# Performance work log

Measured on AMD Instinct MI355X. Metric: run time of the kernel, lower is better.

Reference implementation:

```python
import jax, jax.numpy as jnp
import numpy as np


def setup_inputs() -> dict:
    key = jax.random.key(0)
    ks = jax.random.split(key, 8)
    B, M, C, H, W = 2, 16, 256, 64, 64
    T = 1024  # transformer_dim
    return {
        "transformer_output": jax.random.normal(ks[0], (B, T), dtype=jnp.float32),
        "residual_maps": jax.random.normal(ks[1], (B, M, C, H, W), dtype=jnp.float32),
        "Wq": jax.random.normal(ks[2], (C, T), dtype=jnp.float32) * 0.02,
        "bq": jnp.zeros((C,), dtype=jnp.float32),
        "Wk": jax.random.normal(ks[3], (C, C), dtype=jnp.float32) * 0.02,
        "bk": jnp.zeros((C,), dtype=jnp.float32),
        "Wv": jax.random.normal(ks[4], (C, C), dtype=jnp.float32) * 0.02,
        "bv": jnp.zeros((C,), dtype=jnp.float32),
    }


def reference(transformer_output, residual_maps, Wq, bq, Wk, bk, Wv, bv):
    # residual_maps: [B, M, C, H, W]; single query per batch element.
    B, M, C, H, W = residual_maps.shape
    scale = C ** (-0.5)
    # Linear query projection: [B, C]
    q = transformer_output @ Wq.T + bq
    # 1x1 conv == per-pixel channel matmul: [B, M, C, H, W]
    keys = jnp.einsum("oc,bmchw->bmohw", Wk, residual_maps) + bk[None, None, :, None, None]
    values = jnp.einsum("oc,bmchw->bmohw", Wv, residual_maps) + bv[None, None, :, None, None]
    # Single-query dot-product scores per (map, pixel): [B, M, H, W]
    scores = jnp.einsum("bc,bmchw->bmhw", q, keys) * scale
    # Temporal softmax over num_maps at each spatial position
    probs = jax.nn.softmax(scores, axis=1)
    # Softmax-weighted sum of value maps: [B, C, H, W]
    out = jnp.einsum("bmhw,bmchw->bchw", probs, values)
    return out
```

## Files before the change

### kernel.cpp

```cpp
#include <hip/hip_runtime.h>

#define SCALE 0.0625f
#define ROW 36

typedef __attribute__((ext_vector_type(4))) float f32x4;
typedef __attribute__((ext_vector_type(8))) short s16x8;
typedef __attribute__((ext_vector_type(8))) unsigned short u16x8;

__device__ __forceinline__ unsigned short f2bf(float x) {
    unsigned u = __float_as_uint(x);
    u = u + 0x7FFF + ((u >> 16) & 1);
    return (unsigned short)(u >> 16);
}

__global__ __launch_bounds__(256) void prep1_kernel(
    const float* __restrict__ TO,
    const float* __restrict__ Wq,
    const float* __restrict__ bq,
    const float* __restrict__ Wv,
    float* __restrict__ qbuf,
    unsigned short* __restrict__ WvB)
{
    const int blk = blockIdx.x;
    const int t   = threadIdx.x;
    if (blk < 16) {
        const int b    = blk >> 3;
        const int rblk = blk & 7;
        const int wv = t >> 6, l = t & 63;
        const float4* Wq4 = (const float4*)Wq;
        const float4* TO4 = (const float4*)TO;
        for (int rr = 0; rr < 8; ++rr) {
            const int c = rblk * 32 + wv * 8 + rr;
            float acc = 0.f;
#pragma unroll
            for (int i = 0; i < 4; ++i) {
                float4 wq = Wq4[c * 256 + i * 64 + l];
                float4 tv = TO4[b * 256 + i * 64 + l];
                acc = fmaf(wq.x, tv.x, acc);
                acc = fmaf(wq.y, tv.y, acc);
                acc = fmaf(wq.z, tv.z, acc);
                acc = fmaf(wq.w, tv.w, acc);
            }
#pragma unroll
            for (int mask = 1; mask < 64; mask <<= 1)
                acc += __shfl_xor(acc, mask, 64);
            if (l == 0) qbuf[b * 256 + c] = acc + bq[c];
        }
    } else {
        const int idx = blk - 16;
#pragma unroll
        for (int i = 0; i < 4; ++i) {
            const int e = idx * 4096 + i * 1024 + t * 4;
            const float4 f = ((const float4*)Wv)[e >> 2];
            ushort4 o;
            o.x = f2bf(f.x); o.y = f2bf(f.y);
            o.z = f2bf(f.z); o.w = f2bf(f.w);
            *(ushort4*)(WvB + e) = o;
        }
    }
}

__global__ __launch_bounds__(256) void prep2_kernel(
    const float* __restrict__ qbuf,
    const float* __restrict__ Wk,
    float* __restrict__ qks)
{
    const int blk = blockIdx.x;
    const int t   = threadIdx.x;
    const int b = blk >> 3, j = blk & 7;
    const int col = t & 31, chunk = t >> 5;
    const int cp = j * 32 + col;
    float partial = 0.f;
#pragma unroll 8
    for (int cc = 0; cc < 32; ++cc) {
        const int c = chunk * 32 + cc;
        partial = fmaf(qbuf[b * 256 + c], Wk[c * 256 + cp], partial);
    }
    __shared__ float r2[8][32];
    r2[chunk][col] = partial;
    __syncthreads();
    if (t < 32) {
        float s = 0.f;
#pragma unroll
        for (int k = 0; k < 8; ++k) s += r2[k][t];
        qks[b * 256 + j * 32 + t] = SCALE * s;
    }
}

__global__ __launch_bounds__(512) void score_kernel(
    const float* __restrict__ X,
    const float* __restrict__ qks,
    float* __restrict__ Sp)
{
    const int blk = blockIdx.x;
    const int ch  = blk & 7;
    const int bm  = blk >> 3;
    const int b   = bm >> 4;
    const int t   = threadIdx.x;
    const int c0  = ch * 32;
    const float4* X4 = (const float4*)X;
    const int base = (bm * 256 + c0) * 1024;

    float4 a0 = make_float4(0.f, 0.f, 0.f, 0.f);
    float4 a1 = make_float4(0.f, 0.f, 0.f, 0.f);
#pragma unroll 4
    for (int c = 0; c < 32; ++c) {
        const float q = qks[b * 256 + c0 + c];
        const float4 x0 = X4[base + c * 1024 + t];
        const float4 x1 = X4[base + c * 1024 + t + 512];
        a0.x = fmaf(q, x0.x, a0.x); a0.y = fmaf(q, x0.y, a0.y);
        a0.z = fmaf(q, x0.z, a0.z); a0.w = fmaf(q, x0.w, a0.w);
        a1.x = fmaf(q, x1.x, a1.x); a1.y = fmaf(q, x1.y, a1.y);
        a1.z = fmaf(q, x1.z, a1.z); a1.w = fmaf(q, x1.w, a1.w);
    }
    float4* S4 = (float4*)(Sp + (ch * 32 + bm) * 4096);
    S4[t]       = a0;
    S4[t + 512] = a1;
}

__global__ __launch_bounds__(128) void softmax_kernel(
    const float* __restrict__ Sp,
    float* __restrict__ P)
{
    const int blk = blockIdx.x;
    const int b   = blk >> 5;
    const int px  = ((blk & 31) << 7) + threadIdx.x;
    float e[16];
    float sum = 0.f;
#pragma unroll
    for (int m = 0; m < 16; ++m) {
        float s = 0.f;
#pragma unroll
        for (int ch = 0; ch < 8; ++ch)
            s += Sp[((ch * 2 + b) * 16 + m) * 4096 + px];
        e[m] = __expf(s);
        sum += e[m];
    }
    const float inv = 1.0f / sum;
#pragma unroll
    for (int m = 0; m < 16; ++m)
        P[(b * 16 + m) * 4096 + px] = e[m] * inv;
}

__global__ __launch_bounds__(512) void wsum_kernel(
    const float* __restrict__ X,
    const float* __restrict__ P,
    unsigned short* __restrict__ Ybf)
{
    const int blk = blockIdx.x;
    const int ph  = blk & 1;
    const int oc  = (blk >> 1) & 63;
    const int b   = blk >> 7;
    const int t   = threadIdx.x;
    const int o0  = oc * 4;
    const int px4 = (ph << 9) + t;
    const float4* X4 = (const float4*)X;
    const float4* P4 = (const float4*)P;

    float4 acc[4];
#pragma unroll
    for (int o = 0; o < 4; ++o) acc[o] = make_float4(0.f, 0.f, 0.f, 0.f);

#pragma unroll 2
    for (int m = 0; m < 16; ++m) {
        const float4 p = P4[(b * 16 + m) * 1024 + px4];
#pragma unroll
        for (int o = 0; o < 4; ++o) {
            const float4 x = X4[((b * 16 + m) * 256 + o0 + o) * 1024 + px4];
            acc[o].x = fmaf(p.x, x.x, acc[o].x);
            acc[o].y = fmaf(p.y, x.y, acc[o].y);
            acc[o].z = fmaf(p.z, x.z, acc[o].z);
            acc[o].w = fmaf(p.w, x.w, acc[o].w);
        }
    }
#pragma unroll
    for (int o = 0; o < 4; ++o) {
        ushort4 y;
        y.x = f2bf(acc[o].x); y.y = f2bf(acc[o].y);
        y.z = f2bf(acc[o].z); y.w = f2bf(acc[o].w);
        *(ushort4*)(Ybf + (b * 256 + o0 + o) * 4096 + px4 * 4) = y;
    }
}

__global__ __launch_bounds__(512) void conv_kernel(
    const unsigned short* __restrict__ Ybf,
    const unsigned short* __restrict__ WvB,
    const float* __restrict__ bv,
    float* __restrict__ out)
{
    const int blk = blockIdx.x;
    const int b   = blk >> 7;
    const int px0 = (blk & 127) << 5;
    const int t   = threadIdx.x;
    const int lane = t & 63;
    const int w    = t >> 6;

    __shared__ float slab[256 * ROW];

    {
        const int o = t >> 2, q = t & 3;
#pragma unroll
        for (int h = 0; h < 2; ++h) {
            const int oo = o + h * 128;
            const u16x8 v = *(const u16x8*)(Ybf + (b * 256 + oo) * 4096 + px0 + q * 8);
#pragma unroll
            for (int j = 0; j < 8; ++j)
                slab[oo * ROW + q * 8 + j] =
                    __uint_as_float((unsigned)(unsigned short)v[j] << 16);
        }
    }
    __syncthreads();

    const int px16 = lane & 15;
    const int quad = lane >> 4;

    f32x4 acc[2][2];
#pragma unroll
    for (int tl = 0; tl < 2; ++tl)
#pragma unroll
        for (int pxh = 0; pxh < 2; ++pxh)
#pragma unroll
            for (int r = 0; r < 4; ++r)
                acc[tl][pxh][r] = bv[16 * (w * 2 + tl) + quad * 4 + r];

#pragma unroll
    for (int ks = 0; ks < 8; ++ks) {
        s16x8 bfr[2];
#pragma unroll
        for (int pxh = 0; pxh < 2; ++pxh)
#pragma unroll
            for (int j = 0; j < 8; ++j)
                bfr[pxh][j] = (short)f2bf(
                    slab[(ks * 32 + quad * 8 + j) * ROW + pxh * 16 + px16]);
#pragma unroll
        for (int tl = 0; tl < 2; ++tl) {
            const s16x8 afr = *(const s16x8*)(
                WvB + (16 * (w * 2 + tl) + px16) * 256 + ks * 32 + quad * 8);
#pragma unroll
            for (int pxh = 0; pxh < 2; ++pxh)
                acc[tl][pxh] = __builtin_amdgcn_mfma_f32_16x16x32_bf16(
                    afr, bfr[pxh], acc[tl][pxh], 0, 0, 0);
        }
    }

    const int obase = b * 256 * 4096 + px0;
#pragma unroll
    for (int tl = 0; tl < 2; ++tl)
#pragma unroll
        for (int pxh = 0; pxh < 2; ++pxh)
#pragma unroll
            for (int r = 0; r < 4; ++r) {
                const int co = 16 * (w * 2 + tl) + quad * 4 + r;
                out[obase + co * 4096 + pxh * 16 + px16] = acc[tl][pxh][r];
            }
}

extern "C" void kernel_launch(void* const* d_in, const int* in_sizes, int n_in,
                              void* d_out, int out_size, void* d_ws, size_t ws_size,
                              hipStream_t stream) {
    const float* TO = (const float*)d_in[0];
    const float* X  = (const float*)d_in[1];
    const float* Wq = (const float*)d_in[2];
    const float* bq = (const float*)d_in[3];
    const float* Wk = (const float*)d_in[4];
    const float* Wv = (const float*)d_in[6];
    const float* bv = (const float*)d_in[7];
    float* out = (float*)d_out;
    float* ws  = (float*)d_ws;

    float*          qbuf = ws;
    float*          qks  = ws + 512;
    unsigned short* WvB  = (unsigned short*)(ws + 1024);
    float*          Sp   = ws + 33792;
    float*          P    = ws + 1082368;
    unsigned short* Ybf  = (unsigned short*)(ws + 1213440);

    hipLaunchKernelGGL(prep1_kernel, dim3(32), dim3(256), 0, stream,
                       TO, Wq, bq, Wv, qbuf, WvB);
    hipLaunchKernelGGL(prep2_kernel, dim3(16), dim3(256), 0, stream,
                       qbuf, Wk, qks);
    hipLaunchKernelGGL(score_kernel, dim3(256), dim3(512), 0, stream,
                       X, qks, Sp);
    hipLaunchKernelGGL(softmax_kernel, dim3(64), dim3(128), 0, stream,
                       Sp, P);
    hipLaunchKernelGGL(wsum_kernel, dim3(256), dim3(512), 0, stream,
                       X, P, Ybf);
    hipLaunchKernelGGL(conv_kernel, dim3(256), dim3(512), 0, stream,
                       Ybf, WvB, bv, out);
}
```

Before: 248.9 us.

## Fuse five stage kernels into one cooperative kernel with grid syncs

Replaces the prep2, score, softmax, wsum and conv launches with a single cooperative kernel of 256 blocks that separates the stages with grid.sync barriers. The softmax stage is also rewritten to use float4 loads and a shuffle reduction over the 16 maps, spread across 32 blocks of 512 threads instead of 64 blocks of 128. This removes per-launch overhead and inter-kernel gaps. In exchange it adds grid-wide barrier costs, leaves most blocks idle during the small stages, and needs all 256 blocks to be co-resident. The large shared slab now sits in every block for the whole kernel, which may limit occupancy.

```diff
diff --git a/kernel.cpp b/kernel.cpp
--- a/kernel.cpp
+++ b/kernel.cpp
@@ -1,4 +1,7 @@
 #include <hip/hip_runtime.h>
+#include <hip/hip_cooperative_groups.h>
+
+namespace cg = cooperative_groups;
 
 #define SCALE 0.0625f
 #define ROW 36
@@ -60,199 +63,206 @@
     }
 }
 
-__global__ __launch_bounds__(256) void prep2_kernel(
+__global__ __launch_bounds__(512, 2) void fused_kernel(
+    const float* __restrict__ X,
     const float* __restrict__ qbuf,
     const float* __restrict__ Wk,
-    float* __restrict__ qks)
-{
-    const int blk = blockIdx.x;
-    const int t   = threadIdx.x;
-    const int b = blk >> 3, j = blk & 7;
-    const int col = t & 31, chunk = t >> 5;
-    const int cp = j * 32 + col;
-    float partial = 0.f;
-#pragma unroll 8
-    for (int cc = 0; cc < 32; ++cc) {
-        const int c = chunk * 32 + cc;
-        partial = fmaf(qbuf[b * 256 + c], Wk[c * 256 + cp], partial);
-    }
-    __shared__ float r2[8][32];
-    r2[chunk][col] = partial;
-    __syncthreads();
-    if (t < 32) {
-        float s = 0.f;
-#pragma unroll
-        for (int k = 0; k < 8; ++k) s += r2[k][t];
-        qks[b * 256 + j * 32 + t] = SCALE * s;
-    }
-}
-
-__global__ __launch_bounds__(512) void score_kernel(
-    const float* __restrict__ X,
-    const float* __restrict__ qks,
-    float* __restrict__ Sp)
-{
-    const int blk = blockIdx.x;
-    const int ch  = blk & 7;
-    const int bm  = blk >> 3;
-    const int b   = bm >> 4;
-    const int t   = threadIdx.x;
-    const int c0  = ch * 32;
-    const float4* X4 = (const float4*)X;
-    const int base = (bm * 256 + c0) * 1024;
-
-    float4 a0 = make_float4(0.f, 0.f, 0.f, 0.f);
-    float4 a1 = make_float4(0.f, 0.f, 0.f, 0.f);
-#pragma unroll 4
-    for (int c = 0; c < 32; ++c) {
-        const float q = qks[b * 256 + c0 + c];
-        const float4 x0 = X4[base + c * 1024 + t];
-        const float4 x1 = X4[base + c * 1024 + t + 512];
-        a0.x = fmaf(q, x0.x, a0.x); a0.y = fmaf(q, x0.y, a0.y);
-        a0.z = fmaf(q, x0.z, a0.z); a0.w = fmaf(q, x0.w, a0.w);
-        a1.x = fmaf(q, x1.x, a1.x); a1.y = fmaf(q, x1.y, a1.y);
-        a1.z = fmaf(q, x1.z, a1.z); a1.w = fmaf(q, x1.w, a1.w);
-    }
-    float4* S4 = (float4*)(Sp + (ch * 32 + bm) * 4096);
-    S4[t]       = a0;
-    S4[t + 512] = a1;
-}
-
-__global__ __launch_bounds__(128) void softmax_kernel(
-    const float* __restrict__ Sp,
-    float* __restrict__ P)
-{
-    const int blk = blockIdx.x;
-    const int b   = blk >> 5;
-    const int px  = ((blk & 31) << 7) + threadIdx.x;
-    float e[16];
-    float sum = 0.f;
-#pragma unroll
-    for (int m = 0; m < 16; ++m) {
-        float s = 0.f;
-#pragma unroll
-        for (int ch = 0; ch < 8; ++ch)
-            s += Sp[((ch * 2 + b) * 16 + m) * 4096 + px];
-        e[m] = __expf(s);
-        sum += e[m];
-    }
-    const float inv = 1.0f / sum;
-#pragma unroll
-    for (int m = 0; m < 16; ++m)
-        P[(b * 16 + m) * 4096 + px] = e[m] * inv;
-}
-
-__global__ __launch_bounds__(512) void wsum_kernel(
-    const float* __restrict__ X,
-    const float* __restrict__ P,
-    unsigned short* __restrict__ Ybf)
-{
-    const int blk = blockIdx.x;
-    const int ph  = blk & 1;
-    const int oc  = (blk >> 1) & 63;
-    const int b   = blk >> 7;
-    const int t   = threadIdx.x;
-    const int o0  = oc * 4;
-    const int px4 = (ph << 9) + t;
-    const float4* X4 = (const float4*)X;
-    const float4* P4 = (const float4*)P;
-
-    float4 acc[4];
-#pragma unroll
-    for (int o = 0; o < 4; ++o) acc[o] = make_float4(0.f, 0.f, 0.f, 0.f);
-
-#pragma unroll 2
-    for (int m = 0; m < 16; ++m) {
-        const float4 p = P4[(b * 16 + m) * 1024 + px4];
-#pragma unroll
-        for (int o = 0; o < 4; ++o) {
-            const float4 x = X4[((b * 16 + m) * 256 + o0 + o) * 1024 + px4];
-            acc[o].x = fmaf(p.x, x.x, acc[o].x);
-            acc[o].y = fmaf(p.y, x.y, acc[o].y);
-            acc[o].z = fmaf(p.z, x.z, acc[o].z);
-            acc[o].w = fmaf(p.w, x.w, acc[o].w);
-        }
-    }
-#pragma unroll
-    for (int o = 0; o < 4; ++o) {
-        ushort4 y;
-        y.x = f2bf(acc[o].x); y.y = f2bf(acc[o].y);
-        y.z = f2bf(acc[o].z); y.w = f2bf(acc[o].w);
-        *(ushort4*)(Ybf + (b * 256 + o0 + o) * 4096 + px4 * 4) = y;
-    }
-}
-
-__global__ __launch_bounds__(512) void conv_kernel(
-    const unsigned short* __restrict__ Ybf,
+    float* __restrict__ qks,
+    float* __restrict__ Sp,
+    float* __restrict__ P,
+    unsigned short* __restrict__ Ybf,
     const unsigned short* __restrict__ WvB,
     const float* __restrict__ bv,
     float* __restrict__ out)
 {
+    cg::grid_group grid = cg::this_grid();
     const int blk = blockIdx.x;
-    const int b   = blk >> 7;
-    const int px0 = (blk & 127) << 5;
     const int t   = threadIdx.x;
-    const int lane = t & 63;
-    const int w    = t >> 6;
 
     __shared__ float slab[256 * ROW];
+    __shared__ float r2[16][32];
+
+    if (blk < 16) {
+        const int b = blk >> 3, j = blk & 7;
+        const int col = t & 31, chunk = t >> 5;
+        const int cp = j * 32 + col;
+        float partial = 0.f;
+#pragma unroll
+        for (int cc = 0; cc < 16; ++cc) {
+            const int c = chunk * 16 + cc;
+            partial = fmaf(qbuf[b * 256 + c], Wk[c * 256 + cp], partial);
+        }
+        r2[chunk][col] = partial;
+        __syncthreads();
+        if (t < 32) {
+            float s = 0.f;
+#pragma unroll
+            for (int k = 0; k < 16; ++k) s += r2[k][t];
+            qks[b * 256 + j * 32 + t] = SCALE * s;
+        }
+    }
+    __threadfence();
+    grid.sync();
 
     {
-        const int o = t >> 2, q = t & 3;
-#pragma unroll
-        for (int h = 0; h < 2; ++h) {
-            const int oo = o + h * 128;
-            const u16x8 v = *(const u16x8*)(Ybf + (b * 256 + oo) * 4096 + px0 + q * 8);
-#pragma unroll
-            for (int j = 0; j < 8; ++j)
-                slab[oo * ROW + q * 8 + j] =
-                    __uint_as_float((unsigned)(unsigned short)v[j] << 16);
-        }
-    }
-    __syncthreads();
-
-    const int px16 = lane & 15;
-    const int quad = lane >> 4;
-
-    f32x4 acc[2][2];
-#pragma unroll
-    for (int tl = 0; tl < 2; ++tl)
-#pragma unroll
-        for (int pxh = 0; pxh < 2; ++pxh)
-#pragma unroll
-            for (int r = 0; r < 4; ++r)
-                acc[tl][pxh][r] = bv[16 * (w * 2 + tl) + quad * 4 + r];
-
-#pragma unroll
-    for (int ks = 0; ks < 8; ++ks) {
-        s16x8 bfr[2];
-#pragma unroll
-        for (int pxh = 0; pxh < 2; ++pxh)
-#pragma unroll
-            for (int j = 0; j < 8; ++j)
-                bfr[pxh][j] = (short)f2bf(
-                    slab[(ks * 32 + quad * 8 + j) * ROW + pxh * 16 + px16]);
-#pragma unroll
-        for (int tl = 0; tl < 2; ++tl) {
-            const s16x8 afr = *(const s16x8*)(
-                WvB + (16 * (w * 2 + tl) + px16) * 256 + ks * 32 + quad * 8);
+        const int ch = blk & 7;
+        const int bm = blk >> 3;
+        const int b  = bm >> 4;
+        const int c0 = ch * 32;
+        const float4* X4 = (const float4*)X;
+        const int base = (bm * 256 + c0) * 1024;
+
+        float4 a0 = make_float4(0.f, 0.f, 0.f, 0.f);
+        float4 a1 = make_float4(0.f, 0.f, 0.f, 0.f);
+#pragma unroll 4
+        for (int c = 0; c < 32; ++c) {
+            const float q = qks[b * 256 + c0 + c];
+            const float4 x0 = X4[base + c * 1024 + t];
+            const float4 x1 = X4[base + c * 1024 + t + 512];
+            a0.x = fmaf(q, x0.x, a0.x); a0.y = fmaf(q, x0.y, a0.y);
+            a0.z = fmaf(q, x0.z, a0.z); a0.w = fmaf(q, x0.w, a0.w);
+            a1.x = fmaf(q, x1.x, a1.x); a1.y = fmaf(q, x1.y, a1.y);
+            a1.z = fmaf(q, x1.z, a1.z); a1.w = fmaf(q, x1.w, a1.w);
+        }
+        float4* S4 = (float4*)(Sp + (ch * 32 + bm) * 4096);
+        S4[t]       = a0;
+        S4[t + 512] = a1;
+    }
+    __threadfence();
+    grid.sync();
+
+    if (blk < 32) {
+        const int b = blk >> 4, g = blk & 15;
+        const int m = t & 15, f4g = t >> 4;
+        const float4* Sp4 = (const float4*)Sp;
+#pragma unroll
+        for (int rep = 0; rep < 2; ++rep) {
+            const int f4c = g * 64 + rep * 32 + f4g;
+            float4 s = make_float4(0.f, 0.f, 0.f, 0.f);
+#pragma unroll
+            for (int ch = 0; ch < 8; ++ch) {
+                const float4 v = Sp4[((ch * 2 + b) * 16 + m) * 1024 + f4c];
+                s.x += v.x; s.y += v.y; s.z += v.z; s.w += v.w;
+            }
+            float4 e;
+            e.x = __expf(s.x); e.y = __expf(s.y);
+            e.z = __expf(s.z); e.w = __expf(s.w);
+            float4 tot = e;
+#pragma unroll
+            for (int mask = 1; mask < 16; mask <<= 1) {
+                tot.x += __shfl_xor(tot.x, mask, 64);
+                tot.y += __shfl_xor(tot.y, mask, 64);
+                tot.z += __shfl_xor(tot.z, mask, 64);
+                tot.w += __shfl_xor(tot.w, mask, 64);
+            }
+            float4 p;
+            p.x = e.x / tot.x; p.y = e.y / tot.y;
+            p.z = e.z / tot.z; p.w = e.w / tot.w;
+            ((float4*)P)[(b * 16 + m) * 1024 + f4c] = p;
+        }
+    }
+    __threadfence();
+    grid.sync();
+
+    {
+        const int ph = blk & 1;
+        const int oc = (blk >> 1) & 63;
+        const int b  = blk >> 7;
+        const int o0 = oc * 4;
+        const int px4 = (ph << 9) + t;
+        const float4* X4 = (const float4*)X;
+        const float4* P4 = (const float4*)P;
+
+        float4 acc[4];
+#pragma unroll
+        for (int o = 0; o < 4; ++o) acc[o] = make_float4(0.f, 0.f, 0.f, 0.f);
+
+#pragma unroll 2
+        for (int m = 0; m < 16; ++m) {
+            const float4 p = P4[(b * 16 + m) * 1024 + px4];
+#pragma unroll
+            for (int o = 0; o < 4; ++o) {
+                const float4 x = X4[((b * 16 + m) * 256 + o0 + o) * 1024 + px4];
+                acc[o].x = fmaf(p.x, x.x, acc[o].x);
+                acc[o].y = fmaf(p.y, x.y, acc[o].y);
+                acc[o].z = fmaf(p.z, x.z, acc[o].z);
+                acc[o].w = fmaf(p.w, x.w, acc[o].w);
+            }
+        }
+#pragma unroll
+        for (int o = 0; o < 4; ++o) {
+            ushort4 y;
+            y.x = f2bf(acc[o].x); y.y = f2bf(acc[o].y);
+            y.z = f2bf(acc[o].z); y.w = f2bf(acc[o].w);
+            *(ushort4*)(Ybf + (b * 256 + o0 + o) * 4096 + px4 * 4) = y;
+        }
+    }
+    __threadfence();
+    grid.sync();
+
+    {
+        const int b   = blk >> 7;
+        const int px0 = (blk & 127) << 5;
+        const int lane = t & 63;
+        const int w    = t >> 6;
+
+        {
+            const int o = t >> 2, q = t & 3;
+#pragma unroll
+            for (int h = 0; h < 2; ++h) {
+                const int oo = o + h * 128;
+                const u16x8 v = *(const u16x8*)(Ybf + (b * 256 + oo) * 4096 + px0 + q * 8);
+#pragma unroll
+                for (int j = 0; j < 8; ++j)
+                    slab[oo * ROW + q * 8 + j] =
+                        __uint_as_float((unsigned)(unsigned short)v[j] << 16);
+            }
+        }
+        __syncthreads();
+
+        const int px16 = lane & 15;
+        const int quad = lane >> 4;
+
+        f32x4 acc[2][2];
+#pragma unroll
+        for (int tl = 0; tl < 2; ++tl)
 #pragma unroll
             for (int pxh = 0; pxh < 2; ++pxh)
-                acc[tl][pxh] = __builtin_amdgcn_mfma_f32_16x16x32_bf16(
-                    afr, bfr[pxh], acc[tl][pxh], 0, 0, 0);
-        }
-    }
-
-    const int obase = b * 256 * 4096 + px0;
-#pragma unroll
-    for (int tl = 0; tl < 2; ++tl)
-#pragma unroll
-        for (int pxh = 0; pxh < 2; ++pxh)
-#pragma unroll
-            for (int r = 0; r < 4; ++r) {
-                const int co = 16 * (w * 2 + tl) + quad * 4 + r;
-                out[obase + co * 4096 + pxh * 16 + px16] = acc[tl][pxh][r];
-            }
+#pragma unroll
+                for (int r = 0; r < 4; ++r)
+                    acc[tl][pxh][r] = bv[16 * (w * 2 + tl) + quad * 4 + r];
+
+#pragma unroll
+        for (int ks = 0; ks < 8; ++ks) {
+            s16x8 bfr[2];
+#pragma unroll
+            for (int pxh = 0; pxh < 2; ++pxh)
+#pragma unroll
+                for (int j = 0; j < 8; ++j)
+                    bfr[pxh][j] = (short)f2bf(
+                        slab[(ks * 32 + quad * 8 + j) * ROW + pxh * 16 + px16]);
+#pragma unroll
+            for (int tl = 0; tl < 2; ++tl) {
+                const s16x8 afr = *(const s16x8*)(
+                    WvB + (16 * (w * 2 + tl) + px16) * 256 + ks * 32 + quad * 8);
+#pragma unroll
+                for (int pxh = 0; pxh < 2; ++pxh)
+                    acc[tl][pxh] = __builtin_amdgcn_mfma_f32_16x16x32_bf16(
+                        afr, bfr[pxh], acc[tl][pxh], 0, 0, 0);
+            }
+        }
+
+        const int obase = b * 256 * 4096 + px0;
+#pragma unroll
+        for (int tl = 0; tl < 2; ++tl)
+#pragma unroll
+            for (int pxh = 0; pxh < 2; ++pxh)
+#pragma unroll
+                for (int r = 0; r < 4; ++r) {
+                    const int co = 16 * (w * 2 + tl) + quad * 4 + r;
+                    out[obase + co * 4096 + pxh * 16 + px16] = acc[tl][pxh][r];
+                }
+    }
 }
 
 extern "C" void kernel_launch(void* const* d_in, const int* in_sizes, int n_in,
@@ -277,14 +287,10 @@
 
     hipLaunchKernelGGL(prep1_kernel, dim3(32), dim3(256), 0, stream,
                        TO, Wq, bq, Wv, qbuf, WvB);
-    hipLaunchKernelGGL(prep2_kernel, dim3(16), dim3(256), 0, stream,
-                       qbuf, Wk, qks);
-    hipLaunchKernelGGL(score_kernel, dim3(256), dim3(512), 0, stream,
-                       X, qks, Sp);
-    hipLaunchKernelGGL(softmax_kernel, dim3(64), dim3(128), 0, stream,
-                       Sp, P);
-    hipLaunchKernelGGL(wsum_kernel, dim3(256), dim3(512), 0, stream,
-                       X, P, Ybf);
-    hipLaunchKernelGGL(conv_kernel, dim3(256), dim3(512), 0, stream,
-                       Ybf, WvB, bv, out);
-}
+
+    void* args[] = {(void*)&X, (void*)&qbuf, (void*)&Wk, (void*)&qks,
+                    (void*)&Sp, (void*)&P, (void*)&Ybf, (void*)&WvB,
+                    (void*)&bv, (void*)&out};
+    hipLaunchCooperativeKernel((const void*)fused_kernel, dim3(256), dim3(512),
+                               args, 0, stream);
+}
```

After: 585.9 us. +135.4%, slower.

## Fuse prep stages, reduce scores in-block, and fold softmax into weighted sum

Applied to the files above, without the earlier changes.

Merges the query projection and Wk folding into one prep kernel that uses shared memory. The score kernel now reduces the channel partials inside each block and writes final scores directly, so the 8x partial-score buffer goes away. Softmax moves into the weighted-sum kernel: each block recomputes the exp and normalisation from the scores, so the softmax launch and the P round trip are removed. This cuts two launches and a lot of intermediate traffic, but the exp work is repeated across the 64 output-channel blocks, and the prep path is now serial in only 2 blocks.

```diff
diff --git a/kernel.cpp b/kernel.cpp
--- a/kernel.cpp
+++ b/kernel.cpp
@@ -13,24 +13,25 @@
     return (unsigned short)(u >> 16);
 }
 
-__global__ __launch_bounds__(256) void prep1_kernel(
+__global__ __launch_bounds__(256) void prep_kernel(
     const float* __restrict__ TO,
     const float* __restrict__ Wq,
     const float* __restrict__ bq,
+    const float* __restrict__ Wk,
     const float* __restrict__ Wv,
-    float* __restrict__ qbuf,
+    float* __restrict__ qks,
     unsigned short* __restrict__ WvB)
 {
     const int blk = blockIdx.x;
     const int t   = threadIdx.x;
-    if (blk < 16) {
-        const int b    = blk >> 3;
-        const int rblk = blk & 7;
+    if (blk < 2) {
+        const int b = blk;
+        __shared__ float sq[256];
         const int wv = t >> 6, l = t & 63;
         const float4* Wq4 = (const float4*)Wq;
         const float4* TO4 = (const float4*)TO;
-        for (int rr = 0; rr < 8; ++rr) {
-            const int c = rblk * 32 + wv * 8 + rr;
+        for (int rr = 0; rr < 64; ++rr) {
+            const int c = wv * 64 + rr;
             float acc = 0.f;
 #pragma unroll
             for (int i = 0; i < 4; ++i) {
@@ -44,10 +45,16 @@
 #pragma unroll
             for (int mask = 1; mask < 64; mask <<= 1)
                 acc += __shfl_xor(acc, mask, 64);
-            if (l == 0) qbuf[b * 256 + c] = acc + bq[c];
-        }
+            if (l == 0) sq[c] = acc + bq[c];
+        }
+        __syncthreads();
+        float val = 0.f;
+#pragma unroll 8
+        for (int c = 0; c < 256; ++c)
+            val = fmaf(sq[c], Wk[c * 256 + t], val);
+        qks[b * 256 + t] = SCALE * val;
     } else {
-        const int idx = blk - 16;
+        const int idx = blk - 2;
 #pragma unroll
         for (int i = 0; i < 4; ++i) {
             const int e = idx * 4096 + i * 1024 + t * 4;
@@ -60,102 +67,78 @@
     }
 }
 
-__global__ __launch_bounds__(256) void prep2_kernel(
-    const float* __restrict__ qbuf,
-    const float* __restrict__ Wk,
-    float* __restrict__ qks)
-{
-    const int blk = blockIdx.x;
-    const int t   = threadIdx.x;
-    const int b = blk >> 3, j = blk & 7;
-    const int col = t & 31, chunk = t >> 5;
-    const int cp = j * 32 + col;
-    float partial = 0.f;
-#pragma unroll 8
-    for (int cc = 0; cc < 32; ++cc) {
-        const int c = chunk * 32 + cc;
-        partial = fmaf(qbuf[b * 256 + c], Wk[c * 256 + cp], partial);
-    }
-    __shared__ float r2[8][32];
-    r2[chunk][col] = partial;
-    __syncthreads();
-    if (t < 32) {
-        float s = 0.f;
-#pragma unroll
-        for (int k = 0; k < 8; ++k) s += r2[k][t];
-        qks[b * 256 + j * 32 + t] = SCALE * s;
-    }
-}
-
-__global__ __launch_bounds__(512) void score_kernel(
+__global__ __launch_bounds__(256, 2) void score_kernel(
     const float* __restrict__ X,
     const float* __restrict__ qks,
-    float* __restrict__ Sp)
-{
-    const int blk = blockIdx.x;
-    const int ch  = blk & 7;
-    const int bm  = blk >> 3;
+    float* __restrict__ S)
+{
+    const int blk = blockIdx.x;
+    const int bm  = blk >> 4;
+    const int pxq = blk & 15;
     const int b   = bm >> 4;
     const int t   = threadIdx.x;
-    const int c0  = ch * 32;
+    const int cg  = t >> 6, f4l = t & 63;
+
     const float4* X4 = (const float4*)X;
-    const int base = (bm * 256 + c0) * 1024;
-
-    float4 a0 = make_float4(0.f, 0.f, 0.f, 0.f);
-    float4 a1 = make_float4(0.f, 0.f, 0.f, 0.f);
-#pragma unroll 4
-    for (int c = 0; c < 32; ++c) {
-        const float q = qks[b * 256 + c0 + c];
-        const float4 x0 = X4[base + c * 1024 + t];
-        const float4 x1 = X4[base + c * 1024 + t + 512];
-        a0.x = fmaf(q, x0.x, a0.x); a0.y = fmaf(q, x0.y, a0.y);
-        a0.z = fmaf(q, x0.z, a0.z); a0.w = fmaf(q, x0.w, a0.w);
-        a1.x = fmaf(q, x1.x, a1.x); a1.y = fmaf(q, x1.y, a1.y);
-        a1.z = fmaf(q, x1.z, a1.z); a1.w = fmaf(q, x1.w, a1.w);
-    }
-    float4* S4 = (float4*)(Sp + (ch * 32 + bm) * 4096);
-    S4[t]       = a0;
-    S4[t + 512] = a1;
-}
-
-__global__ __launch_bounds__(128) void softmax_kernel(
-    const float* __restrict__ Sp,
-    float* __restrict__ P)
-{
-    const int blk = blockIdx.x;
-    const int b   = blk >> 5;
-    const int px  = ((blk & 31) << 7) + threadIdx.x;
-    float e[16];
-    float sum = 0.f;
+    const int base = (bm * 256 + cg * 64) * 1024 + pxq * 64 + f4l;
+    const float* q = qks + b * 256 + cg * 64;
+
+    float4 a = make_float4(0.f, 0.f, 0.f, 0.f);
+#pragma unroll 8
+    for (int cc = 0; cc < 64; ++cc) {
+        const float4 x = X4[base + cc * 1024];
+        const float qv = q[cc];
+        a.x = fmaf(qv, x.x, a.x);
+        a.y = fmaf(qv, x.y, a.y);
+        a.z = fmaf(qv, x.z, a.z);
+        a.w = fmaf(qv, x.w, a.w);
+    }
+    __shared__ float4 part[4][64];
+    part[cg][f4l] = a;
+    __syncthreads();
+    if (t < 64) {
+        const float4 s0 = part[0][t], s1 = part[1][t];
+        const float4 s2 = part[2][t], s3 = part[3][t];
+        float4 r;
+        r.x = s0.x + s1.x + s2.x + s3.x;
+        r.y = s0.y + s1.y + s2.y + s3.y;
+        r.z = s0.z + s1.z + s2.z + s3.z;
+        r.w = s0.w + s1.w + s2.w + s3.w;
+        ((float4*)S)[bm * 1024 + pxq * 64 + t] = r;
+    }
+}
+
+__global__ __launch_bounds__(256, 2) void wsum_kernel(
+    const float* __restrict__ X,
+    const float* __restrict__ S,
+    unsigned short* __restrict__ Ybf)
+{
+    const int blk = blockIdx.x;
+    const int pxq = blk & 3;
+    const int oc  = (blk >> 2) & 63;
+    const int b   = blk >> 8;
+    const int t   = threadIdx.x;
+    const int px4 = pxq * 256 + t;
+    const int o0  = oc * 4;
+    const float4* X4 = (const float4*)X;
+    const float4* S4 = (const float4*)S;
+
+    float4 p[16];
+    float4 tot = make_float4(0.f, 0.f, 0.f, 0.f);
 #pragma unroll
     for (int m = 0; m < 16; ++m) {
-        float s = 0.f;
-#pragma unroll
-        for (int ch = 0; ch < 8; ++ch)
-            s += Sp[((ch * 2 + b) * 16 + m) * 4096 + px];
-        e[m] = __expf(s);
-        sum += e[m];
-    }
-    const float inv = 1.0f / sum;
-#pragma unroll
-    for (int m = 0; m < 16; ++m)
-        P[(b * 16 + m) * 4096 + px] = e[m] * inv;
-}
-
-__global__ __launch_bounds__(512) void wsum_kernel(
-    const float* __restrict__ X,
-    const float* __restrict__ P,
-    unsigned short* __restrict__ Ybf)
-{
-    const int blk = blockIdx.x;
-    const int ph  = blk & 1;
-    const int oc  = (blk >> 1) & 63;
-    const int b   = blk >> 7;
-    const int t   = threadIdx.x;
-    const int o0  = oc * 4;
-    const int px4 = (ph << 9) + t;
-    const float4* X4 = (const float4*)X;
-    const float4* P4 = (const float4*)P;
+        const float4 s = S4[(b * 16 + m) * 1024 + px4];
+        p[m].x = __expf(s.x); p[m].y = __expf(s.y);
+        p[m].z = __expf(s.z); p[m].w = __expf(s.w);
+        tot.x += p[m].x; tot.y += p[m].y;
+        tot.z += p[m].z; tot.w += p[m].w;
+    }
+    const float ix = 1.0f / tot.x, iy = 1.0f / tot.y;
+    const float iz = 1.0f / tot.z, iw = 1.0f / tot.w;
+#pragma unroll
+    for (int m = 0; m < 16; ++m) {
+        p[m].x *= ix; p[m].y *= iy; p[m].z *= iz; p[m].w *= iw;
+    }
 
     float4 acc[4];
 #pragma unroll
@@ -163,14 +146,14 @@
 
 #pragma unroll 2
     for (int m = 0; m < 16; ++m) {
-        const float4 p = P4[(b * 16 + m) * 1024 + px4];
+        const float4 pm = p[m];
 #pragma unroll
         for (int o = 0; o < 4; ++o) {
             const float4 x = X4[((b * 16 + m) * 256 + o0 + o) * 1024 + px4];
-            acc[o].x = fmaf(p.x, x.x, acc[o].x);
-            acc[o].y = fmaf(p.y, x.y, acc[o].y);
-            acc[o].z = fmaf(p.z, x.z, acc[o].z);
-            acc[o].w = fmaf(p.w, x.w, acc[o].w);
+            acc[o].x = fmaf(pm.x, x.x, acc[o].x);
+            acc[o].y = fmaf(pm.y, x.y, acc[o].y);
+            acc[o].z = fmaf(pm.z, x.z, acc[o].z);
+            acc[o].w = fmaf(pm.w, x.w, acc[o].w);
         }
     }
 #pragma unroll
@@ -268,23 +251,17 @@
     float* out = (float*)d_out;
     float* ws  = (float*)d_ws;
 
-    float*          qbuf = ws;
-    float*          qks  = ws + 512;
-    unsigned short* WvB  = (unsigned short*)(ws + 1024);
-    float*          Sp   = ws + 33792;
-    float*          P    = ws + 1082368;
-    unsigned short* Ybf  = (unsigned short*)(ws + 1213440);
-
-    hipLaunchKernelGGL(prep1_kernel, dim3(32), dim3(256), 0, stream,
-                       TO, Wq, bq, Wv, qbuf, WvB);
-    hipLaunchKernelGGL(prep2_kernel, dim3(16), dim3(256), 0, stream,
-                       qbuf, Wk, qks);
-    hipLaunchKernelGGL(score_kernel, dim3(256), dim3(512), 0, stream,
-                       X, qks, Sp);
-    hipLaunchKernelGGL(softmax_kernel, dim3(64), dim3(128), 0, stream,
-                       Sp, P);
-    hipLaunchKernelGGL(wsum_kernel, dim3(256), dim3(512), 0, stream,
-                       X, P, Ybf);
+    float*          qks = ws;
+    unsigned short* WvB = (unsigned short*)(ws + 512);
+    float*          S   = ws + 33280;
+    unsigned short* Ybf = (unsigned short*)(ws + 164352);
+
+    hipLaunchKernelGGL(prep_kernel, dim3(18), dim3(256), 0, stream,
+                       TO, Wq, bq, Wk, Wv, qks, WvB);
+    hipLaunchKernelGGL(score_kernel, dim3(512), dim3(256), 0, stream,
+                       X, qks, S);
+    hipLaunchKernelGGL(wsum_kernel, dim3(512), dim3(256), 0, stream,
+                       X, S, Ybf);
     hipLaunchKernelGGL(conv_kernel, dim3(256), dim3(512), 0, stream,
                        Ybf, WvB, bv, out);
 }
```

Result: slower. 323.6 us (+30.0%).
